# Kernel tuning notes

Hardware: AMD Instinct MI355X
Metric: run time of the kernel (lower is better)

Reference implementation:

```python
import jax, jax.numpy as jnp
import numpy as np

N, D = 8192, 128

def _rbf_kernel(x, y):
    # InfoVAE-style kernel: exp(-mean((x_i - y_j)^2) / dim) = exp(-sqdist / dim^2)
    dim = x.shape[1]
    x2 = jnp.sum(x * x, axis=1)              # [n]
    y2 = jnp.sum(y * y, axis=1)              # [m]
    sqdist = x2[:, None] + y2[None, :] - 2.0 * (x @ y.T)  # [n, m]
    return jnp.exp(-sqdist / (dim * dim))


def setup_inputs() -> dict:
    key = jax.random.key(0)
    k1, k2 = jax.random.split(key)
    inputs = jax.random.normal(k1, (N, D), dtype=jnp.float32)
    true_samples = jax.random.normal(k2, (N, D), dtype=jnp.float32)
    return {"inputs": inputs, "true_samples": true_samples}


def reference(inputs, true_samples):
    x = true_samples  # samples from standard normal prior
    y = inputs
    k_xx = _rbf_kernel(x, x)
    k_yy = _rbf_kernel(y, y)
    k_xy = _rbf_kernel(x, y)
    mmd = jnp.mean(k_xx) + jnp.mean(k_yy) - 2.0 * jnp.mean(k_xy)
    return mmd
```

## Files before the change

kernel.cpp:

```cpp
#include <hip/hip_runtime.h>
#include <hip/hip_bf16.h>
#include <math.h>


#define NN 8192
#define DD 128
#define TZ 16384
#define TILES 128
#define NBLOCKS (TILES * (TILES + 1) / 2)

typedef __attribute__((ext_vector_type(8))) short bf16x8;
typedef __attribute__((ext_vector_type(4))) float f32x4;
typedef __attribute__((ext_vector_type(2))) float f32x2;

#if __has_builtin(__builtin_amdgcn_exp2f)
#define EXP2F __builtin_amdgcn_exp2f
#else
#define EXP2F exp2f
#endif

constexpr float LOG2E = 0x1.715476p+0f;
constexpr float S2 = LOG2E / 8192.0f;

constexpr int PANEL = 16384;

constexpr size_t WS_NORM = 768;
constexpr size_t WS_Z    = WS_NORM + (size_t)TZ * sizeof(float);

__device__ __forceinline__ void gload_lds16(const void* g, void* l) {
  __builtin_amdgcn_global_load_lds(
      (const __attribute__((address_space(1))) void*)g,
      (__attribute__((address_space(3))) void*)l, 16, 0, 0);
}

__global__ __launch_bounds__(256) void prep(
    const float* __restrict__ X, const float* __restrict__ Y,
    __hip_bfloat16* __restrict__ Z, float* __restrict__ normZ,
    double* __restrict__ sums) {
  if (blockIdx.x == 0 && threadIdx.x < 64) sums[threadIdx.x] = 0.0;

  const int row = blockIdx.x * 4 + (threadIdx.x >> 6);
  const int lane = threadIdx.x & 63;
  const float* __restrict__ src =
      (row < NN) ? (X + (size_t)row * DD) : (Y + (size_t)(row - NN) * DD);
  const float2 v = *reinterpret_cast<const float2*>(src + 2 * lane);

  float n = v.x * v.x + v.y * v.y;
  *reinterpret_cast<__hip_bfloat162*>(Z + (size_t)row * DD + 2 * lane) =
      __hip_bfloat162{__float2bfloat16(v.x), __float2bfloat16(v.y)};

#pragma unroll
  for (int o = 32; o > 0; o >>= 1) n += __shfl_down(n, o);
  if (lane == 0) normZ[row] = n * (-LOG2E / 16384.0f);
}

__device__ __forceinline__ int tri_start(int i) {
  return i * TILES - (i * (i - 1)) / 2;
}

__global__ __launch_bounds__(256, 4) void mmd_mfma(
    const __hip_bfloat16* __restrict__ Z, const float* __restrict__ normZ,
    double* __restrict__ sums) {
  __shared__ alignas(16) char lds[2 * PANEL + 1024];
  __shared__ float rowN[128], colN[128];
  __shared__ double red[4];

  const int t = blockIdx.x;
  int I = (int)((257.0 - sqrt(257.0 * 257.0 - 8.0 * (double)t)) * 0.5);
  if (I > 127) I = 127;
  if (I < 0) I = 0;
  while (I < 127 && tri_start(I + 1) <= t) ++I;
  while (I > 0 && tri_start(I) > t) --I;
  const int J = I + (t - tri_start(I));

  const int tid = threadIdx.x;
  const int lane = tid & 63, wave = tid >> 6;
  const int wr = wave >> 1, wc = wave & 1;
  const int lr = lane & 15, quad = lane >> 4;

  if (tid < 128) rowN[tid] = normZ[I * 128 + tid];
  else           colN[tid - 128] = normZ[J * 128 + tid - 128];

  const char* Zb = (const char*)Z;
  const int r5 = tid >> 3;
  const int g = (tid & 7) ^ (r5 & 7);
  const char* gA = Zb + (size_t)I * 32768 + r5 * 256 + g * 16;
  const char* gB = Zb + (size_t)J * 32768 + r5 * 256 + g * 16;
  char* lw = lds + wave * 1024;

  const int aBase = (wr * 64 + lr) * 128;
  const int bBase = PANEL + (wc * 64 + lr) * 128;
  const int sa = lr & 7;

  f32x4 acc[4][4] = {};
#pragma unroll
  for (int p = 0; p < 2; ++p) {
    __syncthreads();
#pragma unroll
    for (int l = 0; l < 4; ++l) {
      gload_lds16(gA + p * 128 + l * 8192, lw + l * 4096);
      gload_lds16(gB + p * 128 + l * 8192, lw + PANEL + l * 4096);
    }
    __syncthreads();

#pragma unroll
    for (int ks = 0; ks < 2; ++ks) {
      const int csw = (((ks * 4) + quad) ^ sa) * 16;
      bf16x8 a[4], b[4];
#pragma unroll
      for (int i = 0; i < 4; ++i) {
        a[i] = *reinterpret_cast<const bf16x8*>(&lds[aBase + i * 2048 + csw]);
        b[i] = *reinterpret_cast<const bf16x8*>(&lds[bBase + i * 2048 + csw]);
      }
#pragma unroll
      for (int i = 0; i < 4; ++i)
#pragma unroll
        for (int j = 0; j < 4; ++j)
          acc[i][j] = __builtin_amdgcn_mfma_f32_16x16x32_bf16(a[i], b[j], acc[i][j], 0, 0, 0);
    }
  }

  const f32x2 s2v = {S2, S2};
  f32x2 part01 = {0.f, 0.f}, part23 = {0.f, 0.f};
#pragma unroll
  for (int i = 0; i < 4; ++i) {
    const int rbase = wr * 64 + i * 16 + quad * 4;
    const f32x2 ar01 = {rowN[rbase + 0], rowN[rbase + 1]};
    const f32x2 ar23 = {rowN[rbase + 2], rowN[rbase + 3]};
#pragma unroll
    for (int j = 0; j < 4; ++j) {
      const float rb = colN[wc * 64 + j * 16 + lr];
      const f32x2 rb2 = {rb, rb};
      const f32x2 base01 = ar01 + rb2;
      const f32x2 base23 = ar23 + rb2;
      const f32x2 acc01 = {acc[i][j][0], acc[i][j][1]};
      const f32x2 acc23 = {acc[i][j][2], acc[i][j][3]};
      const f32x2 arg01 = __builtin_elementwise_fma(acc01, s2v, base01);
      const f32x2 arg23 = __builtin_elementwise_fma(acc23, s2v, base23);
      part01 += (f32x2){EXP2F(arg01.x), EXP2F(arg01.y)};
      part23 += (f32x2){EXP2F(arg23.x), EXP2F(arg23.y)};
    }
  }
  const f32x2 ps = part01 + part23;
  double local = (double)(ps.x + ps.y);
  double w = ((I < 64) == (J < 64)) ? 1.0 : -1.0;
  if (I != J) w += w;
  local *= w;

#pragma unroll
  for (int o = 32; o > 0; o >>= 1) local += __shfl_down(local, o);
  if (lane == 0) red[wave] = local;
  __syncthreads();
  if (tid == 0) atomicAdd(&sums[t & 63], red[0] + red[1] + red[2] + red[3]);
}

__global__ void finish(const double* __restrict__ s, float* __restrict__ out) {
  double v = s[threadIdx.x];
#pragma unroll
  for (int o = 32; o > 0; o >>= 1) v += __shfl_down(v, o);
  if (threadIdx.x == 0)
    out[0] = (float)(v * (1.0 / ((double)NN * (double)NN)));
}

extern "C" void kernel_launch(void* const* d_in, const int* in_sizes, int n_in,
                              void* d_out, int out_size, void* d_ws, size_t ws_size,
                              hipStream_t stream) {
  const float* y_inputs = (const float*)d_in[0];
  const float* x_true   = (const float*)d_in[1];
  float* out = (float*)d_out;

  char* ws = (char*)d_ws;
  double* sums = (double*)ws;
  float* normZ = (float*)(ws + WS_NORM);
  __hip_bfloat16* Z = (__hip_bfloat16*)(ws + WS_Z);

  prep<<<TZ / 4, 256, 0, stream>>>(x_true, y_inputs, Z, normZ, sums);
  mmd_mfma<<<NBLOCKS, 256, 0, stream>>>(Z, normZ, sums);
  finish<<<1, 64, 0, stream>>>(sums, out);
}
```

Measured before the change: 110.3 us.

## Use persistent blocks over tile ranges, reuse A panel, fuse final reduction

Replaces one-block-per-tile launch with 768 persistent blocks that each walk 10-11 consecutive upper-triangular tiles. The full 128x128 A row panel stays in LDS while J advances, and B fragments are read straight from global memory into registers. The separate finish kernel is removed: the last block to arrive, tracked by an atomic counter, does the final reduction. This cuts launch and per-tile setup costs and reloads of A, at the cost of uncached B reads from global/L2 and lower occupancy.

```diff
diff --git a/kernel.cpp b/kernel.cpp
--- a/kernel.cpp
+++ b/kernel.cpp
@@ -7,7 +7,8 @@
 #define DD 128
 #define TZ 16384
 #define TILES 128
-#define NBLOCKS (TILES * (TILES + 1) / 2)
+#define NTILES (TILES * (TILES + 1) / 2)
+#define GRID 768
 
 typedef __attribute__((ext_vector_type(8))) short bf16x8;
 typedef __attribute__((ext_vector_type(4))) float f32x4;
@@ -22,8 +23,7 @@
 constexpr float LOG2E = 0x1.715476p+0f;
 constexpr float S2 = LOG2E / 8192.0f;
 
-constexpr int PANEL = 16384;
-
+constexpr size_t WS_CTR  = 512;
 constexpr size_t WS_NORM = 768;
 constexpr size_t WS_Z    = WS_NORM + (size_t)TZ * sizeof(float);
 
@@ -36,8 +36,11 @@
 __global__ __launch_bounds__(256) void prep(
     const float* __restrict__ X, const float* __restrict__ Y,
     __hip_bfloat16* __restrict__ Z, float* __restrict__ normZ,
-    double* __restrict__ sums) {
-  if (blockIdx.x == 0 && threadIdx.x < 64) sums[threadIdx.x] = 0.0;
+    double* __restrict__ sums, unsigned* __restrict__ ctr) {
+  if (blockIdx.x == 0) {
+    if (threadIdx.x < 64) sums[threadIdx.x] = 0.0;
+    if (threadIdx.x == 64) *ctr = 0u;
+  }
 
   const int row = blockIdx.x * 4 + (threadIdx.x >> 6);
   const int lane = threadIdx.x & 63;
@@ -58,108 +61,137 @@
   return i * TILES - (i * (i - 1)) / 2;
 }
 
-__global__ __launch_bounds__(256, 4) void mmd_mfma(
+__global__ __launch_bounds__(256, 3) void mmd_mfma(
     const __hip_bfloat16* __restrict__ Z, const float* __restrict__ normZ,
-    double* __restrict__ sums) {
-  __shared__ alignas(16) char lds[2 * PANEL + 1024];
-  __shared__ float rowN[128], colN[128];
+    double* __restrict__ sums, unsigned* __restrict__ ctr,
+    float* __restrict__ out) {
+  __shared__ alignas(16) char ldsA[32768];
   __shared__ double red[4];
-
-  const int t = blockIdx.x;
-  int I = (int)((257.0 - sqrt(257.0 * 257.0 - 8.0 * (double)t)) * 0.5);
+  __shared__ bool amLast;
+
+  const int b = blockIdx.x;
+  const int t0 = b * 10 + min(b, 576);
+  const int nt = (b < 576) ? 11 : 10;
+
+  int I = (int)((257.0 - sqrt(257.0 * 257.0 - 8.0 * (double)t0)) * 0.5);
   if (I > 127) I = 127;
   if (I < 0) I = 0;
-  while (I < 127 && tri_start(I + 1) <= t) ++I;
-  while (I > 0 && tri_start(I) > t) --I;
-  const int J = I + (t - tri_start(I));
+  while (I < 127 && tri_start(I + 1) <= t0) ++I;
+  while (I > 0 && tri_start(I) > t0) --I;
+  int J = I + (t0 - tri_start(I));
 
   const int tid = threadIdx.x;
   const int lane = tid & 63, wave = tid >> 6;
   const int wr = wave >> 1, wc = wave & 1;
   const int lr = lane & 15, quad = lane >> 4;
 
-  if (tid < 128) rowN[tid] = normZ[I * 128 + tid];
-  else           colN[tid - 128] = normZ[J * 128 + tid - 128];
-
   const char* Zb = (const char*)Z;
-  const int r5 = tid >> 3;
-  const int g = (tid & 7) ^ (r5 & 7);
-  const char* gA = Zb + (size_t)I * 32768 + r5 * 256 + g * 16;
-  const char* gB = Zb + (size_t)J * 32768 + r5 * 256 + g * 16;
-  char* lw = lds + wave * 1024;
-
-  const int aBase = (wr * 64 + lr) * 128;
-  const int bBase = PANEL + (wc * 64 + lr) * 128;
-  const int sa = lr & 7;
-
-  f32x4 acc[4][4] = {};
-#pragma unroll
-  for (int p = 0; p < 2; ++p) {
-    __syncthreads();
-#pragma unroll
-    for (int l = 0; l < 4; ++l) {
-      gload_lds16(gA + p * 128 + l * 8192, lw + l * 4096);
-      gload_lds16(gB + p * 128 + l * 8192, lw + PANEL + l * 4096);
+
+  const int rowlow = wave * 4 + quad;
+  const int gOffA = rowlow * 256 + ((lane & 15) ^ rowlow) * 16;
+  char* ldsW = ldsA + wave * 1024;
+
+  const int aBase = (wr * 64 + lr) * 256;
+  const int aSw = lr;
+
+  double local = 0.0;
+  bool needA = true;
+  f32x2 ar01[4], ar23[4];
+  const f32x2 s2v = {S2, S2};
+
+  for (int it = 0; it < nt; ++it) {
+    const char* pB = Zb + (size_t)(J * 128 + wc * 64 + lr) * 256 + quad * 16;
+    float cn[4];
+#pragma unroll
+    for (int j = 0; j < 4; ++j) cn[j] = normZ[J * 128 + wc * 64 + j * 16 + lr];
+
+    if (needA) {
+      __syncthreads();
+#pragma unroll
+      for (int k = 0; k < 8; ++k)
+        gload_lds16(Zb + (size_t)I * 32768 + k * 4096 + gOffA,
+                    ldsW + k * 4096);
+#pragma unroll
+      for (int i = 0; i < 4; ++i) {
+        const float* p = normZ + I * 128 + wr * 64 + i * 16 + quad * 4;
+        const float2 v01 = *reinterpret_cast<const float2*>(p);
+        const float2 v23 = *reinterpret_cast<const float2*>(p + 2);
+        ar01[i] = (f32x2){v01.x, v01.y};
+        ar23[i] = (f32x2){v23.x, v23.y};
+      }
+      needA = false;
+      __syncthreads();
     }
-    __syncthreads();
-
-#pragma unroll
-    for (int ks = 0; ks < 2; ++ks) {
-      const int csw = (((ks * 4) + quad) ^ sa) * 16;
-      bf16x8 a[4], b[4];
-#pragma unroll
-      for (int i = 0; i < 4; ++i) {
-        a[i] = *reinterpret_cast<const bf16x8*>(&lds[aBase + i * 2048 + csw]);
-        b[i] = *reinterpret_cast<const bf16x8*>(&lds[bBase + i * 2048 + csw]);
+
+    f32x4 acc[4][4] = {};
+#pragma unroll
+    for (int p = 0; p < 2; ++p) {
+      bf16x8 bq[2][4];
+#pragma unroll
+      for (int ks = 0; ks < 2; ++ks)
+#pragma unroll
+        for (int j = 0; j < 4; ++j)
+          bq[ks][j] = *reinterpret_cast<const bf16x8*>(
+              pB + j * 4096 + p * 128 + ks * 64);
+#pragma unroll
+      for (int ks = 0; ks < 2; ++ks) {
+        const int csw = ((p * 8 + ks * 4 + quad) ^ aSw) * 16;
+        bf16x8 a[4];
+#pragma unroll
+        for (int i = 0; i < 4; ++i)
+          a[i] = *reinterpret_cast<const bf16x8*>(&ldsA[aBase + i * 4096 + csw]);
+#pragma unroll
+        for (int i = 0; i < 4; ++i)
+#pragma unroll
+          for (int j = 0; j < 4; ++j)
+            acc[i][j] = __builtin_amdgcn_mfma_f32_16x16x32_bf16(
+                a[i], bq[ks][j], acc[i][j], 0, 0, 0);
       }
-#pragma unroll
-      for (int i = 0; i < 4; ++i)
-#pragma unroll
-        for (int j = 0; j < 4; ++j)
-          acc[i][j] = __builtin_amdgcn_mfma_f32_16x16x32_bf16(a[i], b[j], acc[i][j], 0, 0, 0);
     }
-  }
-
-  const f32x2 s2v = {S2, S2};
-  f32x2 part01 = {0.f, 0.f}, part23 = {0.f, 0.f};
-#pragma unroll
-  for (int i = 0; i < 4; ++i) {
-    const int rbase = wr * 64 + i * 16 + quad * 4;
-    const f32x2 ar01 = {rowN[rbase + 0], rowN[rbase + 1]};
-    const f32x2 ar23 = {rowN[rbase + 2], rowN[rbase + 3]};
-#pragma unroll
-    for (int j = 0; j < 4; ++j) {
-      const float rb = colN[wc * 64 + j * 16 + lr];
-      const f32x2 rb2 = {rb, rb};
-      const f32x2 base01 = ar01 + rb2;
-      const f32x2 base23 = ar23 + rb2;
-      const f32x2 acc01 = {acc[i][j][0], acc[i][j][1]};
-      const f32x2 acc23 = {acc[i][j][2], acc[i][j][3]};
-      const f32x2 arg01 = __builtin_elementwise_fma(acc01, s2v, base01);
-      const f32x2 arg23 = __builtin_elementwise_fma(acc23, s2v, base23);
-      part01 += (f32x2){EXP2F(arg01.x), EXP2F(arg01.y)};
-      part23 += (f32x2){EXP2F(arg23.x), EXP2F(arg23.y)};
+
+    f32x2 part01 = {0.f, 0.f}, part23 = {0.f, 0.f};
+#pragma unroll
+    for (int i = 0; i < 4; ++i) {
+#pragma unroll
+      for (int j = 0; j < 4; ++j) {
+        const f32x2 rb2 = {cn[j], cn[j]};
+        const f32x2 base01 = ar01[i] + rb2;
+        const f32x2 base23 = ar23[i] + rb2;
+        const f32x2 acc01 = {acc[i][j][0], acc[i][j][1]};
+        const f32x2 acc23 = {acc[i][j][2], acc[i][j][3]};
+        const f32x2 arg01 = __builtin_elementwise_fma(acc01, s2v, base01);
+        const f32x2 arg23 = __builtin_elementwise_fma(acc23, s2v, base23);
+        part01 += (f32x2){EXP2F(arg01.x), EXP2F(arg01.y)};
+        part23 += (f32x2){EXP2F(arg23.x), EXP2F(arg23.y)};
+      }
     }
-  }
-  const f32x2 ps = part01 + part23;
-  double local = (double)(ps.x + ps.y);
-  double w = ((I < 64) == (J < 64)) ? 1.0 : -1.0;
-  if (I != J) w += w;
-  local *= w;
+    const f32x2 ps = part01 + part23;
+    double w = ((I < 64) == (J < 64)) ? 1.0 : -1.0;
+    if (I != J) w += w;
+    local += w * (double)(ps.x + ps.y);
+
+    ++J;
+    if (J >= TILES) { ++I; J = I; needA = true; }
+  }
 
 #pragma unroll
   for (int o = 32; o > 0; o >>= 1) local += __shfl_down(local, o);
   if (lane == 0) red[wave] = local;
   __syncthreads();
-  if (tid == 0) atomicAdd(&sums[t & 63], red[0] + red[1] + red[2] + red[3]);
-}
-
-__global__ void finish(const double* __restrict__ s, float* __restrict__ out) {
-  double v = s[threadIdx.x];
-#pragma unroll
-  for (int o = 32; o > 0; o >>= 1) v += __shfl_down(v, o);
-  if (threadIdx.x == 0)
-    out[0] = (float)(v * (1.0 / ((double)NN * (double)NN)));
+  if (tid == 0) {
+    atomicAdd(&sums[b & 63], red[0] + red[1] + red[2] + red[3]);
+    __threadfence();
+    const unsigned prev = atomicAdd(ctr, 1u);
+    amLast = (prev == GRID - 1);
+  }
+  __syncthreads();
+  if (amLast && wave == 0) {
+    double v = atomicAdd(&sums[lane], 0.0);
+#pragma unroll
+    for (int o = 32; o > 0; o >>= 1) v += __shfl_down(v, o);
+    if (lane == 0)
+      out[0] = (float)(v * (1.0 / ((double)NN * (double)NN)));
+  }
 }
 
 extern "C" void kernel_launch(void* const* d_in, const int* in_sizes, int n_in,
@@ -171,10 +203,10 @@
 
   char* ws = (char*)d_ws;
   double* sums = (double*)ws;
+  unsigned* ctr = (unsigned*)(ws + WS_CTR);
   float* normZ = (float*)(ws + WS_NORM);
   __hip_bfloat16* Z = (__hip_bfloat16*)(ws + WS_Z);
 
-  prep<<<TZ / 4, 256, 0, stream>>>(x_true, y_inputs, Z, normZ, sums);
-  mmd_mfma<<<NBLOCKS, 256, 0, stream>>>(Z, normZ, sums);
-  finish<<<1, 64, 0, stream>>>(sums, out);
-}
+  prep<<<TZ / 4, 256, 0, stream>>>(x_true, y_inputs, Z, normZ, sums, ctr);
+  mmd_mfma<<<GRID, 256, 0, stream>>>(Z, normZ, sums, ctr, out);
+}
```

Result: slower. 132.6 us (+20.2%).
